# Kernel tuning notes

Measured on AMD Instinct MI355X. Metric: run time of the kernel, lower is better.

## Reference

```python
import jax, jax.numpy as jnp
import numpy as np

# BT.601-style conversion matrices (c_new = A @ c_old on column vectors)
RGB2YUV = jnp.array([[0.299, 0.587, 0.114],
                     [-0.14713, -0.28886, 0.436],
                     [0.615, -0.51499, -0.10001]], dtype=jnp.float32)
YUV2RGB = jnp.array([[1.0, 0.0, 1.13983],
                     [1.0, -0.39465, -0.58060],
                     [1.0, 2.03211, 0.0]], dtype=jnp.float32)

LUM_K = 3     # neighbor_sz
CHROM_K = 9   # int(neighbor_sz * color_sigma_ratio) = int(3*3)
N_ITER = 1


def median_filter2d(x, k):
    """Sliding-window 2D median over the last two dims of x [..., H, W].
    Matches scipy.ndimage.median_filter(size=k, mode='reflect'), i.e.
    numpy 'symmetric' padding, centered odd window."""
    H, W = x.shape[-2], x.shape[-1]
    p = k // 2
    pad = [(0, 0)] * (x.ndim - 2) + [(p, p), (p, p)]
    xp = jnp.pad(x, pad, mode='symmetric')
    # stack k*k shifted views -> [..., H, W, k*k]
    windows = jnp.stack([xp[..., i:i + H, j:j + W]
                         for i in range(k) for j in range(k)], axis=-1)
    return jnp.median(windows, axis=-1)


def setup_inputs() -> dict:
    key = jax.random.key(0)
    image = jax.random.uniform(key, (4, 3, 512, 512), dtype=jnp.float32)
    return {"image": image}


def reference(image):
    # rgb -> yuv
    yuv = jnp.einsum('ij,kjlm->kilm', RGB2YUV, image)
    for _ in range(N_ITER):
        lum = yuv[:, 0:1]
        out_lum = jnp.clip(median_filter2d(lum, LUM_K), 0.0, 1.0)
        out_chrom = median_filter2d(yuv[:, 1:3], CHROM_K)
        yuv = jnp.concatenate([out_lum, out_chrom], axis=1)
    # yuv -> rgb
    return jnp.einsum('ij,kjlm->kilm', YUV2RGB, yuv)
```

## Files before the change

### kernel.cpp

```cpp
#include <hip/hip_runtime.h>
#include <stdint.h>

namespace {

constexpr int H = 512, W = 512;
constexpr int PLANE = H * W;
constexpr int IMG3 = 3 * PLANE;

constexpr float U_LO = -0.436f, U_HI = 0.436f;
constexpr float V_LO = -0.615f, V_HI = 0.615f;
constexpr float NBINS = 64.0f;

constexpr int TW = 64, TH = 16;
constexpr int CW = 72, CH = 24;
constexpr int US = 19;
constexpr int LUMS = 73;

__device__ __forceinline__ int refl(int i, int n) {
    i = (i < 0) ? (-1 - i) : i;
    return (i >= n) ? (2 * n - 1 - i) : i;
}
__device__ __forceinline__ void cas(float& a, float& b) {
    float t = fminf(a, b); b = fmaxf(a, b); a = t;
}
__device__ __forceinline__ float med3(float a, float b, float c) {
    return fmaxf(fminf(a, b), fminf(fmaxf(a, b), c));
}

__device__ __forceinline__ uint32_t fsh(uint32_t w1, uint32_t w0, uint32_t sh) {
    return (uint32_t)(((((uint64_t)w1) << 32) | w0) >> sh);
}

__device__ __forceinline__ uint32_t sadacc(uint32_t t, uint32_t acc) {
#if __has_builtin(__builtin_amdgcn_sad_u8)
    return __builtin_amdgcn_sad_u8(t, 0u, acc);
#else
    return acc + (t >> 7);
#endif
}
__device__ __forceinline__ uint32_t cntscaled(uint32_t acc) {
#if __has_builtin(__builtin_amdgcn_sad_u8)
    return acc;
#else
    return ((acc * 0x01010101u) >> 24) << 7;
#endif
}

__device__ __forceinline__ uint32_t permb(uint32_t hi, uint32_t lo, uint32_t sel) {
#if __has_builtin(__builtin_amdgcn_perm)
    return __builtin_amdgcn_perm(hi, lo, sel);
#else
    uint32_t r = 0;
#pragma unroll
    for (int b = 0; b < 4; ++b) {
        uint32_t s = (sel >> (8 * b)) & 7u;
        uint32_t byte = ((s < 4u) ? (lo >> (8 * s)) : (hi >> (8 * (s - 4u)))) & 0xFFu;
        r |= byte << (8 * b);
    }
    return r;
#endif
}

__device__ __forceinline__ uint32_t coarse_bin16(uint32_t ELo, uint32_t EHi,
                                                 uint32_t OLo, uint32_t OHi) {
    uint32_t w0 = permb(EHi, ELo, 0x05010400u);
    uint32_t w1 = permb(EHi, ELo, 0x07030602u);
    uint32_t w2 = permb(OHi, OLo, 0x05010400u);
    uint32_t w3 = permb(OHi, OLo, 0x07030602u);
    uint32_t c0 = w0 + (w0 << 8); c0 += c0 << 16;
    uint32_t c1 = w1 + (w1 << 8); c1 += c1 << 16;
    uint32_t c2 = w2 + (w2 << 8); c2 += c2 << 16;
    uint32_t c3 = w3 + (w3 << 8); c3 += c3 << 16;
    uint32_t t = (c0 >> 24) * 0x01010101u;
    c1 += t;
    t = (c1 >> 24) * 0x01010101u;
    c2 += t;
    t = (c2 >> 24) * 0x01010101u;
    c3 += t;
    uint32_t f0 = (0xA8A8A8A8u - c0) & 0x80808080u;
    uint32_t f1 = (0xA8A8A8A8u - c1) & 0x80808080u;
    uint32_t f2 = (0xA8A8A8A8u - c2) & 0x80808080u;
    uint32_t f3 = (0xA8A8A8A8u - c3) & 0x80808080u;
    uint32_t s = sadacc(f3, sadacc(f2, sadacc(f1, sadacc(f0, 0u))));
    return cntscaled(s) >> 7;
}

__device__ __forceinline__ void buildP(const uint32_t* rw, uint32_t sh, uint32_t* P) {
    uint32_t p01 = 0, p1 = 0, p2v = 0;
#pragma unroll
    for (int r = 0; r < 9; ++r) {
        uint32_t w0 = rw[3 * r], w1 = rw[3 * r + 1], w2 = rw[3 * r + 2];
        P[2 * r]     = fsh(w1, w0, sh);
        P[2 * r + 1] = fsh(w2, w1, sh);
        uint32_t l = (w2 >> sh) & 0xFFu;
        if (r < 4)      p01 |= l << (8 * r);
        else if (r < 8) p1  |= l << (8 * (r - 4));
        else            p2v = l;
    }
    P[18] = p01; P[19] = p1; P[20] = p2v;
}

__device__ __forceinline__ void fine2(const uint32_t* __restrict__ P0,
                                      const uint32_t* __restrict__ P1,
                                      uint32_t b0, uint32_t b1,
                                      uint32_t& k0, uint32_t& k1) {
    uint32_t lo0 = b0 << 2, lo1 = b1 << 2;
    uint32_t t0 = (lo0 + 1u) * 0x01010101u;
    uint32_t t1 = (lo1 + 1u) * 0x01010101u;
    uint32_t c0 = t0 + 0x80808080u, c1 = t1 + 0x80808080u;
    const uint32_t T = 44u * 128u;
#pragma unroll
    for (int s = 2; s >= 1; s >>= 1) {
        uint32_t a0 = 0, a1 = 0;
#pragma unroll
        for (int i = 0; i < 21; ++i) {
            a0 = sadacc((c0 - P0[i]) & 0x80808080u, a0);
            a1 = sadacc((c1 - P1[i]) & 0x80808080u, a1);
        }
        bool r0 = cntscaled(a0) < T;
        bool r1 = cntscaled(a1) < T;
        lo0 += r0 ? (uint32_t)s : 0u;
        lo1 += r1 ? (uint32_t)s : 0u;
        if (s > 1) {
            const uint32_t d = 0x01010101u;
            c0 = r0 ? c0 + d : c0 - d;
            c1 = r1 ? c1 + d : c1 - d;
        }
    }
    k0 = lo0; k1 = lo1;
}

__global__ __launch_bounds__(256, 4) void denoise_kernel(const float* __restrict__ img,
                                                         float* __restrict__ out) {
    __shared__ uint32_t uP[CH * US];
    __shared__ uint32_t vP[CH * US];
    __shared__ float lumT[CH * LUMS];
    __shared__ uint32_t histT[2][16][72][2];

    const int tid = threadIdx.x;
    const int tx = tid & 15, ty = tid >> 4;
    const int bx = blockIdx.x, by = blockIdx.y, bz = blockIdx.z;
    const float* __restrict__ base = img + (size_t)bz * IMG3;

    uint8_t* u8p = (uint8_t*)uP;
    uint8_t* v8p = (uint8_t*)vP;

    {
        int idx = tid;
#pragma unroll 7
        for (int it = 0; it < 7; ++it) {
            if (idx < CW * CH) {
                int r = idx / CW, c = idx - r * CW;
                int gy = refl(by * TH + r - 4, H);
                int gx = refl(bx * TW + c - 4, W);
                int o = gy * W + gx;
                float R = base[o], G = base[o + PLANE], B = base[o + 2 * PLANE];
                float Y = 0.299f * R + 0.587f * G + 0.114f * B;
                float U = -0.14713f * R - 0.28886f * G + 0.436f * B;
                float V = 0.615f * R - 0.51499f * G - 0.10001f * B;
                int ku = (int)((U - U_LO) * (NBINS / (U_HI - U_LO)));
                int kv = (int)((V - V_LO) * (NBINS / (V_HI - V_LO)));
                ku = min(max(ku, 0), 63);
                kv = min(max(kv, 0), 63);
                lumT[r * LUMS + c] = Y;
                u8p[r * (US * 4) + c] = (uint8_t)ku;
                v8p[r * (US * 4) + c] = (uint8_t)kv;
            }
            idx += 256;
        }
    }
    __syncthreads();

    if (tid < 144) {
        int ch = (tid >= 72) ? 1 : 0;
        int x = tid - ch * 72;
        const uint8_t* p = (ch ? v8p : u8p) + x;
        uint32_t h0 = 0, h1 = 0;
#pragma unroll
        for (int r = 0; r < 9; ++r) {
            uint32_t b = p[76 * r] >> 2;
            uint32_t d = 1u << ((b & 7u) << 2);
            if (b & 8u) h1 += d; else h0 += d;
        }
        histT[ch][0][x][0] = h0;
        histT[ch][0][x][1] = h1;
        for (int i = 1; i < 16; ++i) {
            uint32_t bo = p[76 * (i - 1)] >> 2;
            uint32_t dob = 1u << ((bo & 7u) << 2);
            if (bo & 8u) h1 -= dob; else h0 -= dob;
            uint32_t bi = p[76 * (i + 8)] >> 2;
            uint32_t dib = 1u << ((bi & 7u) << 2);
            if (bi & 8u) h1 += dib; else h0 += dib;
            histT[ch][i][x][0] = h0;
            histT[ch][i][x][1] = h1;
        }
    }
    __syncthreads();

    uint32_t bins[2][4];
    const uint32_t NM = 0x0F0F0F0Fu;
#pragma unroll
    for (int ch = 0; ch < 2; ++ch) {
        const uint32_t* hrow = &histT[ch][ty][4 * tx][0];
        uint32_t sEL = 0, sEH = 0, sOL = 0, sOH = 0;
#pragma unroll
        for (int c = 3; c <= 8; ++c) {
            uint32_t h0 = hrow[2 * c], h1 = hrow[2 * c + 1];
            sEL += h0 & NM; sEH += (h0 >> 4) & NM;
            sOL += h1 & NM; sOH += (h1 >> 4) & NM;
        }
        uint32_t EL[6], EH[6], OL[6], OH[6];
#pragma unroll
        for (int j = 0; j < 6; ++j) {
            int c = (j < 3) ? j : (j + 6);
            uint32_t h0 = hrow[2 * c], h1 = hrow[2 * c + 1];
            EL[j] = h0 & NM; EH[j] = (h0 >> 4) & NM;
            OL[j] = h1 & NM; OH[j] = (h1 >> 4) & NM;
        }
        bins[ch][0] = coarse_bin16(sEL + EL[0] + EL[1] + EL[2],
                                   sEH + EH[0] + EH[1] + EH[2],
                                   sOL + OL[0] + OL[1] + OL[2],
                                   sOH + OH[0] + OH[1] + OH[2]);
        bins[ch][1] = coarse_bin16(sEL + EL[1] + EL[2] + EL[3],
                                   sEH + EH[1] + EH[2] + EH[3],
                                   sOL + OL[1] + OL[2] + OL[3],
                                   sOH + OH[1] + OH[2] + OH[3]);
        bins[ch][2] = coarse_bin16(sEL + EL[2] + EL[3] + EL[4],
                                   sEH + EH[2] + EH[3] + EH[4],
                                   sOL + OL[2] + OL[3] + OL[4],
                                   sOH + OH[2] + OH[3] + OH[4]);
        bins[ch][3] = coarse_bin16(sEL + EL[3] + EL[4] + EL[5],
                                   sEH + EH[3] + EH[4] + EH[5],
                                   sOL + OL[3] + OL[4] + OL[5],
                                   sOH + OH[3] + OH[4] + OH[5]);
    }

    uint32_t kk[2][4];
#pragma unroll
    for (int ch = 0; ch < 2; ++ch) {
        const uint32_t* plane = ch ? vP : uP;
        uint32_t rw[27];
#pragma unroll
        for (int r = 0; r < 9; ++r) {
            const uint32_t* row = plane + (ty + r) * US + tx;
            rw[3 * r] = row[0]; rw[3 * r + 1] = row[1]; rw[3 * r + 2] = row[2];
        }
        uint32_t P0[21], P1[21];
        buildP(rw, 0u, P0);
        buildP(rw, 8u, P1);
        fine2(P0, P1, bins[ch][0], bins[ch][1], kk[ch][0], kk[ch][1]);
        buildP(rw, 16u, P0);
        buildP(rw, 24u, P1);
        fine2(P0, P1, bins[ch][2], bins[ch][3], kk[ch][2], kk[ch][3]);
    }

    float Ym[4];
    {
        const float* lp = &lumT[(ty + 3) * LUMS + 4 * tx + 3];
        float lo[6], mi[6], hi[6];
#pragma unroll
        for (int j = 0; j < 6; ++j) {
            float a = lp[j], b = lp[j + LUMS], c = lp[j + 2 * LUMS];
            cas(a, b); cas(b, c); cas(a, b);
            lo[j] = a; mi[j] = b; hi[j] = c;
        }
#pragma unroll
        for (int p = 0; p < 4; ++p) {
            float mx = fmaxf(fmaxf(lo[p], lo[p + 1]), lo[p + 2]);
            float md = med3(mi[p], mi[p + 1], mi[p + 2]);
            float mn = fminf(fminf(hi[p], hi[p + 1]), hi[p + 2]);
            Ym[p] = fminf(fmaxf(med3(mx, md, mn), 0.0f), 1.0f);
        }
    }

    const float us = (U_HI - U_LO) / NBINS, vs = (V_HI - V_LO) / NBINS;
    float4 Rq, Gq, Bq;
    float* Rp = &Rq.x; float* Gp = &Gq.x; float* Bp = &Bq.x;
#pragma unroll
    for (int p = 0; p < 4; ++p) {
        float Um = U_LO + ((float)kk[0][p] + 0.5f) * us;
        float Vm = V_LO + ((float)kk[1][p] + 0.5f) * vs;
        Rp[p] = Ym[p] + 1.13983f * Vm;
        Gp[p] = Ym[p] - 0.39465f * Um - 0.5806f * Vm;
        Bp[p] = Ym[p] + 2.03211f * Um;
    }
    size_t o = (size_t)bz * IMG3 + (size_t)(by * TH + ty) * W + (bx * TW + 4 * tx);
    *(float4*)(out + o) = Rq;
    *(float4*)(out + o + PLANE) = Gq;
    *(float4*)(out + o + 2 * PLANE) = Bq;
}

}

extern "C" void kernel_launch(void* const* d_in, const int* in_sizes, int n_in,
                              void* d_out, int out_size, void* d_ws, size_t ws_size,
                              hipStream_t stream) {
    const float* img = (const float*)d_in[0];
    float* out = (float*)d_out;
    int batch = in_sizes[0] / IMG3;
    dim3 grid(W / TW, H / TH, batch);
    dim3 block(256);
    hipLaunchKernelGGL(denoise_kernel, grid, block, 0, stream, img, out);
}
```

Before: 82.14 us.

## Fuse fine median search over four pixels and vectorize interior tile loads

The fine-bin search for the 9x9 chroma median now handles all four output pixels of a thread at once. It masks the shared row words directly instead of building shifted per-pixel packed arrays with 64-bit funnel shifts. Because padding bytes are no longer counted, the threshold drops from 44 to 41, and far fewer SAD operations and shifts run per pixel. Interior tiles load RGB with float4 reads and write packed bin words instead of per-pixel reflected scalar loads. Histogram rows are read as 128-bit LDS loads. This adds code size and register pressure, and a second load path for border tiles.

Result: no change. 82.49 us (+0.4%).

```diff
diff --git a/kernel.cpp b/kernel.cpp
--- a/kernel.cpp
+++ b/kernel.cpp
@@ -25,10 +25,6 @@
 }
 __device__ __forceinline__ float med3(float a, float b, float c) {
     return fmaxf(fminf(a, b), fminf(fmaxf(a, b), c));
-}
-
-__device__ __forceinline__ uint32_t fsh(uint32_t w1, uint32_t w0, uint32_t sh) {
-    return (uint32_t)(((((uint64_t)w1) << 32) | w0) >> sh);
 }
 
 __device__ __forceinline__ uint32_t sadacc(uint32_t t, uint32_t acc) {
@@ -85,49 +81,55 @@
     return cntscaled(s) >> 7;
 }
 
-__device__ __forceinline__ void buildP(const uint32_t* rw, uint32_t sh, uint32_t* P) {
-    uint32_t p01 = 0, p1 = 0, p2v = 0;
-#pragma unroll
-    for (int r = 0; r < 9; ++r) {
-        uint32_t w0 = rw[3 * r], w1 = rw[3 * r + 1], w2 = rw[3 * r + 2];
-        P[2 * r]     = fsh(w1, w0, sh);
-        P[2 * r + 1] = fsh(w2, w1, sh);
-        uint32_t l = (w2 >> sh) & 0xFFu;
-        if (r < 4)      p01 |= l << (8 * r);
-        else if (r < 8) p1  |= l << (8 * (r - 4));
-        else            p2v = l;
-    }
-    P[18] = p01; P[19] = p1; P[20] = p2v;
-}
-
-__device__ __forceinline__ void fine2(const uint32_t* __restrict__ P0,
-                                      const uint32_t* __restrict__ P1,
-                                      uint32_t b0, uint32_t b1,
-                                      uint32_t& k0, uint32_t& k1) {
-    uint32_t lo0 = b0 << 2, lo1 = b1 << 2;
-    uint32_t t0 = (lo0 + 1u) * 0x01010101u;
-    uint32_t t1 = (lo1 + 1u) * 0x01010101u;
-    uint32_t c0 = t0 + 0x80808080u, c1 = t1 + 0x80808080u;
-    const uint32_t T = 44u * 128u;
+__device__ __forceinline__ void fine4(const uint32_t* __restrict__ rw,
+                                      const uint32_t* __restrict__ bins4,
+                                      uint32_t* __restrict__ kk) {
+    uint32_t lo0 = bins4[0] << 2, lo1 = bins4[1] << 2;
+    uint32_t lo2 = bins4[2] << 2, lo3 = bins4[3] << 2;
+    uint32_t c0 = (lo0 + 1u) * 0x01010101u + 0x80808080u;
+    uint32_t c1 = (lo1 + 1u) * 0x01010101u + 0x80808080u;
+    uint32_t c2 = (lo2 + 1u) * 0x01010101u + 0x80808080u;
+    uint32_t c3 = (lo3 + 1u) * 0x01010101u + 0x80808080u;
+    const uint32_t T = 41u * 128u;
+    const uint32_t M0_1 = 0x80808000u, M0_2 = 0x80800000u, M0_3 = 0x80000000u;
+    const uint32_t M2_0 = 0x00000080u, M2_1 = 0x00008080u, M2_2 = 0x00808080u;
 #pragma unroll
     for (int s = 2; s >= 1; s >>= 1) {
-        uint32_t a0 = 0, a1 = 0;
-#pragma unroll
-        for (int i = 0; i < 21; ++i) {
-            a0 = sadacc((c0 - P0[i]) & 0x80808080u, a0);
-            a1 = sadacc((c1 - P1[i]) & 0x80808080u, a1);
-        }
-        bool r0 = cntscaled(a0) < T;
-        bool r1 = cntscaled(a1) < T;
+        uint32_t a0 = 0, a1 = 0, a2 = 0, a3 = 0;
+        uint32_t b0 = 0, b1 = 0, b2 = 0, b3 = 0;
+#pragma unroll
+        for (int r = 0; r < 9; ++r) {
+            uint32_t w0 = rw[3 * r], w1 = rw[3 * r + 1], w2 = rw[3 * r + 2];
+            a0 = sadacc((c0 - w0) & 0x80808080u, a0);
+            a1 = sadacc((c1 - w0) & M0_1, a1);
+            a2 = sadacc((c2 - w0) & M0_2, a2);
+            a3 = sadacc((c3 - w0) & M0_3, a3);
+            b0 = sadacc((c0 - w1) & 0x80808080u, b0);
+            b1 = sadacc((c1 - w1) & 0x80808080u, b1);
+            b2 = sadacc((c2 - w1) & 0x80808080u, b2);
+            b3 = sadacc((c3 - w1) & 0x80808080u, b3);
+            a0 = sadacc((c0 - w2) & M2_0, a0);
+            a1 = sadacc((c1 - w2) & M2_1, a1);
+            a2 = sadacc((c2 - w2) & M2_2, a2);
+            a3 = sadacc((c3 - w2) & 0x80808080u, a3);
+        }
+        bool r0 = cntscaled(a0 + b0) < T;
+        bool r1 = cntscaled(a1 + b1) < T;
+        bool r2 = cntscaled(a2 + b2) < T;
+        bool r3 = cntscaled(a3 + b3) < T;
         lo0 += r0 ? (uint32_t)s : 0u;
         lo1 += r1 ? (uint32_t)s : 0u;
+        lo2 += r2 ? (uint32_t)s : 0u;
+        lo3 += r3 ? (uint32_t)s : 0u;
         if (s > 1) {
             const uint32_t d = 0x01010101u;
             c0 = r0 ? c0 + d : c0 - d;
             c1 = r1 ? c1 + d : c1 - d;
-        }
-    }
-    k0 = lo0; k1 = lo1;
+            c2 = r2 ? c2 + d : c2 - d;
+            c3 = r3 ? c3 + d : c3 - d;
+        }
+    }
+    kk[0] = lo0; kk[1] = lo1; kk[2] = lo2; kk[3] = lo3;
 }
 
 __global__ __launch_bounds__(256, 4) void denoise_kernel(const float* __restrict__ img,
@@ -135,7 +137,7 @@
     __shared__ uint32_t uP[CH * US];
     __shared__ uint32_t vP[CH * US];
     __shared__ float lumT[CH * LUMS];
-    __shared__ uint32_t histT[2][16][72][2];
+    __shared__ __align__(16) uint32_t histT[2][16][72][2];
 
     const int tid = threadIdx.x;
     const int tx = tid & 15, ty = tid >> 4;
@@ -145,7 +147,41 @@
     uint8_t* u8p = (uint8_t*)uP;
     uint8_t* v8p = (uint8_t*)vP;
 
-    {
+    const bool interior = (bx >= 1) && (bx <= 6) && (by >= 1) && (by <= 30);
+    if (interior) {
+        int unit = tid;
+#pragma unroll 2
+        for (int it = 0; it < 2; ++it, unit += 256) {
+            if (unit < 18 * CH) {
+                int r = unit / 18, u = unit - r * 18;
+                const float* p0 = base + (size_t)((by * TH + r - 4) * W + (bx * TW + 4 * u - 4));
+                float4 Rv = *(const float4*)p0;
+                float4 Gv = *(const float4*)(p0 + PLANE);
+                float4 Bv = *(const float4*)(p0 + 2 * PLANE);
+                const float* Rf = &Rv.x; const float* Gf = &Gv.x; const float* Bf = &Bv.x;
+                uint32_t kuw = 0, kvw = 0;
+                float Yq[4];
+#pragma unroll
+                for (int j = 0; j < 4; ++j) {
+                    float R = Rf[j], G = Gf[j], B = Bf[j];
+                    float Y = 0.299f * R + 0.587f * G + 0.114f * B;
+                    float U = -0.14713f * R - 0.28886f * G + 0.436f * B;
+                    float V = 0.615f * R - 0.51499f * G - 0.10001f * B;
+                    int ku = (int)((U - U_LO) * (NBINS / (U_HI - U_LO)));
+                    int kv = (int)((V - V_LO) * (NBINS / (V_HI - V_LO)));
+                    ku = min(max(ku, 0), 63);
+                    kv = min(max(kv, 0), 63);
+                    kuw |= (uint32_t)ku << (8 * j);
+                    kvw |= (uint32_t)kv << (8 * j);
+                    Yq[j] = Y;
+                }
+                uP[r * US + u] = kuw;
+                vP[r * US + u] = kvw;
+                float* lrow = &lumT[r * LUMS + 4 * u];
+                lrow[0] = Yq[0]; lrow[1] = Yq[1]; lrow[2] = Yq[2]; lrow[3] = Yq[3];
+            }
+        }
+    } else {
         int idx = tid;
 #pragma unroll 7
         for (int it = 0; it < 7; ++it) {
@@ -202,10 +238,17 @@
 #pragma unroll
     for (int ch = 0; ch < 2; ++ch) {
         const uint32_t* hrow = &histT[ch][ty][4 * tx][0];
+        uint32_t hw[24];
+#pragma unroll
+        for (int k = 0; k < 6; ++k) {
+            uint4 q = *reinterpret_cast<const uint4*>(hrow + 4 * k);
+            hw[4 * k] = q.x; hw[4 * k + 1] = q.y;
+            hw[4 * k + 2] = q.z; hw[4 * k + 3] = q.w;
+        }
         uint32_t sEL = 0, sEH = 0, sOL = 0, sOH = 0;
 #pragma unroll
         for (int c = 3; c <= 8; ++c) {
-            uint32_t h0 = hrow[2 * c], h1 = hrow[2 * c + 1];
+            uint32_t h0 = hw[2 * c], h1 = hw[2 * c + 1];
             sEL += h0 & NM; sEH += (h0 >> 4) & NM;
             sOL += h1 & NM; sOH += (h1 >> 4) & NM;
         }
@@ -213,7 +256,7 @@
 #pragma unroll
         for (int j = 0; j < 6; ++j) {
             int c = (j < 3) ? j : (j + 6);
-            uint32_t h0 = hrow[2 * c], h1 = hrow[2 * c + 1];
+            uint32_t h0 = hw[2 * c], h1 = hw[2 * c + 1];
             EL[j] = h0 & NM; EH[j] = (h0 >> 4) & NM;
             OL[j] = h1 & NM; OH[j] = (h1 >> 4) & NM;
         }
@@ -245,13 +288,7 @@
             const uint32_t* row = plane + (ty + r) * US + tx;
             rw[3 * r] = row[0]; rw[3 * r + 1] = row[1]; rw[3 * r + 2] = row[2];
         }
-        uint32_t P0[21], P1[21];
-        buildP(rw, 0u, P0);
-        buildP(rw, 8u, P1);
-        fine2(P0, P1, bins[ch][0], bins[ch][1], kk[ch][0], kk[ch][1]);
-        buildP(rw, 16u, P0);
-        buildP(rw, 24u, P1);
-        fine2(P0, P1, bins[ch][2], bins[ch][3], kk[ch][2], kk[ch][3]);
+        fine4(rw, bins[ch], kk[ch]);
     }
 
     float Ym[4];
```
